# Kernel optimization log

Hardware: AMD Instinct MI355X
Metric: run time of the kernel (lower is better)

## Reference

```python
import jax, jax.numpy as jnp
import numpy as np

B, S, E = 2, 2048, 1024
N_HEADS = 16
HEAD_DIM = E // N_HEADS  # 64
ATTN_SCALE = 1.0 / np.sqrt(E)  # NOTE: original scales by 1/sqrt(hidden_dim_phi), not head_dim
ROPE_BASE = 10000.0


def _rope(t):
    # t: (B, H, S, D) with D = HEAD_DIM; interleaved-pair RoPE (torchtune-style)
    d = t.shape[-1]
    s = t.shape[-2]
    inv_freq = 1.0 / (ROPE_BASE ** (jnp.arange(0, d, 2, dtype=jnp.float32) / d))  # (D/2,)
    ang = jnp.arange(s, dtype=jnp.float32)[:, None] * inv_freq[None, :]  # (S, D/2)
    cos, sin = jnp.cos(ang), jnp.sin(ang)  # (S, D/2)
    tp = t.reshape(t.shape[:-1] + (d // 2, 2))
    te, to = tp[..., 0], tp[..., 1]  # (B,H,S,D/2)
    oe = te * cos - to * sin
    oo = te * sin + to * cos
    return jnp.stack([oe, oo], axis=-1).reshape(t.shape)


def setup_inputs() -> dict:
    key = jax.random.key(0)
    ks = jax.random.split(key, 5)
    std = 0.02
    return {
        "x": jax.random.normal(ks[0], (B, S, E), dtype=jnp.float32),
        "W_q": jax.random.normal(ks[1], (E, E), dtype=jnp.float32) * std,
        "W_k": jax.random.normal(ks[2], (E, E), dtype=jnp.float32) * std,
        "W_v": jax.random.normal(ks[3], (E, E), dtype=jnp.float32) * std,
        "W_o": jax.random.normal(ks[4], (E, E), dtype=jnp.float32) * std,
    }


def reference(x, W_q, W_k, W_v, W_o):
    b, s, e = x.shape
    hd = e // N_HEADS
    # projections -> (B, H, S, D)
    def proj(w):
        return (x @ w).reshape(b, s, N_HEADS, hd).transpose(0, 2, 1, 3)
    q = _rope(proj(W_q))
    k = _rope(proj(W_k))
    v = proj(W_v)
    scores = jnp.einsum('bhsd,bhtd->bhst', q, k) * ATTN_SCALE  # (B,H,S,S)
    causal = jnp.triu(jnp.ones((s, s), dtype=bool), k=1)
    scores = jnp.where(causal, -jnp.inf, scores)
    probs = jax.nn.softmax(scores, axis=-1)  # dropout is identity in eval mode
    out = jnp.einsum('bhst,bhtd->bhsd', probs, v)
    out = out.transpose(0, 2, 1, 3).reshape(b, s, e)
    return out @ W_o
```

## Files before the change

### kernel.cpp

```cpp
#include <hip/hip_runtime.h>
#include <hip/hip_bf16.h>

#define S_LEN 2048
#define E_DIM 1024
#define NH 16
#define HD 64
#define ATTN_SCALE 0.03125f
#define QSCALE_L2E 0.045084312f
#define KVB 128

typedef __attribute__((ext_vector_type(8))) short short8;
typedef __attribute__((ext_vector_type(8))) unsigned short ushort8;
typedef __attribute__((ext_vector_type(4))) unsigned short ushort4_t;
typedef __attribute__((ext_vector_type(4))) float f32x4;
typedef __attribute__((ext_vector_type(4))) float f4;
typedef __attribute__((ext_vector_type(2))) unsigned int uint2_t;

__device__ __forceinline__ float bf2f(unsigned short u) {
    unsigned int x = ((unsigned int)u) << 16;
    return __builtin_bit_cast(float, x);
}
__device__ __forceinline__ unsigned short f2bf(float f) {
    unsigned int x = __builtin_bit_cast(unsigned int, f);
    x += 0x7FFFu + ((x >> 16) & 1u);
    return (unsigned short)(x >> 16);
}
__device__ __forceinline__ float exp2_fast(float x) {
    float r;
    asm("v_exp_f32 %0, %1" : "=v"(r) : "v"(x));
    return r;
}
__device__ __forceinline__ void gload16(const unsigned short* g, unsigned short* l) {
    __builtin_amdgcn_global_load_lds(
        (__attribute__((address_space(1))) void*)g,
        (__attribute__((address_space(3))) void*)l, 16, 0, 0);
}

__global__ __launch_bounds__(256) void k_convert(const float* __restrict__ x,
                                                 unsigned short* __restrict__ xb) {
    size_t i = ((size_t)blockIdx.x * 256 + threadIdx.x) * 8;
    f4 a = *(const f4*)(x + i);
    f4 b = *(const f4*)(x + i + 4);
    ushort8 o;
    o[0] = f2bf(a[0]); o[1] = f2bf(a[1]); o[2] = f2bf(a[2]); o[3] = f2bf(a[3]);
    o[4] = f2bf(b[0]); o[5] = f2bf(b[1]); o[6] = f2bf(b[2]); o[7] = f2bf(b[3]);
    *(ushort8*)(xb + i) = o;
}

__global__ __launch_bounds__(256) void k_transw(const float* W0, const float* W1,
                                                const float* W2, const float* W3,
                                                unsigned short* T0, unsigned short* T1,
                                                unsigned short* T2, unsigned short* T3) {
    const float* W; unsigned short* T;
    switch (blockIdx.z) {
        case 0: W = W0; T = T0; break;
        case 1: W = W1; T = T1; break;
        case 2: W = W2; T = T2; break;
        default: W = W3; T = T3; break;
    }
    __shared__ float tile[32][33];
    int tx = threadIdx.x, ty = threadIdx.y;
    int bx = blockIdx.x * 32, by = blockIdx.y * 32;
#pragma unroll
    for (int i = 0; i < 4; i++)
        tile[ty + i * 8][tx] = W[(size_t)(by + ty + i * 8) * E_DIM + bx + tx];
    __syncthreads();
#pragma unroll
    for (int i = 0; i < 4; i++)
        T[(size_t)(bx + ty + i * 8) * E_DIM + by + tx] = f2bf(tile[tx][ty + i * 8]);
}

__global__ __launch_bounds__(256) void k_rope_table(float* __restrict__ cosT,
                                                    float* __restrict__ sinT) {
    int idx = blockIdx.x * 256 + threadIdx.x;
    int s = idx >> 5, j = idx & 31;
    float inv = expf(-(float)j * (9.210340371976184f / 32.f));
    float ang = (float)s * inv;
    cosT[idx] = cosf(ang);
    sinT[idx] = sinf(ang);
}

__global__ __launch_bounds__(256, 3)
void k_gemm97(const unsigned short* __restrict__ A,
              const unsigned short* __restrict__ B,
              unsigned short* __restrict__ Qo,
              unsigned short* __restrict__ Ko,
              unsigned short* __restrict__ Vto,
              const float* __restrict__ cosT,
              const float* __restrict__ sinT) {
    constexpr int NBN = 24;
    constexpr int NWG = 32 * NBN;
    __shared__ unsigned short Alds[4096];
    __shared__ unsigned short Blds[4096];
    int tid = threadIdx.x, lane = tid & 63, wid = tid >> 6;
    int l15 = lane & 15, lg = lane >> 4;
    int wr = wid >> 1, wc = wid & 1;
    int orig = blockIdx.y * NBN + blockIdx.x;
    int wg = (orig & 7) * (NWG / 8) + (orig >> 3);
    int bm = wg / NBN, bn = wg % NBN;
    int c0 = wid * 2, c1c = wid * 2 + 1;
    int srow0 = c0 * 16 + (lane >> 2);
    int srow1 = c1c * 16 + (lane >> 2);
    int scol = (lane & 3) * 8;
    const unsigned short* As0 = A + (size_t)(bm * 128 + srow0) * E_DIM + scol;
    const unsigned short* As1 = A + (size_t)(bm * 128 + srow1) * E_DIM + scol;
    const unsigned short* Bs0 = B + (size_t)(bn * 128 + srow0) * E_DIM + scol;
    const unsigned short* Bs1 = B + (size_t)(bn * 128 + srow1) * E_DIM + scol;
    unsigned short* Ad0 = Alds + c0 * 512;
    unsigned short* Ad1 = Alds + c1c * 512;
    unsigned short* Bd0 = Blds + c0 * 512;
    unsigned short* Bd1 = Blds + c1c * 512;
    f32x4 acc[4][4] = {};
    for (int k0 = 0; k0 < E_DIM; k0 += 32) {
        gload16(As0 + k0, Ad0);
        gload16(As1 + k0, Ad1);
        gload16(Bs0 + k0, Bd0);
        gload16(Bs1 + k0, Bd1);
        __syncthreads();
        short8 af[4], bfr[4];
#pragma unroll
        for (int mf = 0; mf < 4; mf++)
            af[mf] = *(const short8*)(Alds + (wr * 64 + mf * 16 + l15) * 32 + lg * 8);
#pragma unroll
        for (int nf = 0; nf < 4; nf++)
            bfr[nf] = *(const short8*)(Blds + (wc * 64 + nf * 16 + l15) * 32 + lg * 8);
#pragma unroll
        for (int mf = 0; mf < 4; mf++)
#pragma unroll
            for (int nf = 0; nf < 4; nf++)
                acc[mf][nf] = __builtin_amdgcn_mfma_f32_16x16x32_bf16(
                    af[mf], bfr[nf], acc[mf][nf], 0, 0, 0);
        __syncthreads();
    }
#pragma unroll
    for (int mf = 0; mf < 4; mf++) {
        int r0 = bm * 128 + wr * 64 + mf * 16 + lg * 4;
#pragma unroll
        for (int nf = 0; nf < 4; nf++) {
            int colg = bn * 128 + wc * 64 + nf * 16 + l15;
            int z = colg >> 10, c1 = colg & 1023;
            if (z == 2) {
                int h = c1 >> 6, d = c1 & 63;
                int bb = r0 >> 11, s = r0 & 2047;
                ushort4_t p;
#pragma unroll
                for (int r = 0; r < 4; r++) p[r] = f2bf(acc[mf][nf][r]);
                *(ushort4_t*)(Vto + (((size_t)((bb * 16 + h) * 64 + d)) << 11) + s) = p;
            } else {
                unsigned short* T = z ? Ko : Qo;
                int dl = c1 & 63, j = dl >> 1;
                float sgn = (dl & 1) ? 1.f : -1.f;
                float scq = z ? 1.f : QSCALE_L2E;
#pragma unroll
                for (int r = 0; r < 4; r++) {
                    int row = r0 + r, s = row & 2047;
                    float c = cosT[s * 32 + j], sn = sinT[s * 32 + j];
                    float v = acc[mf][nf][r];
                    float p = __shfl_xor(v, 1);
                    T[(size_t)row * E_DIM + c1] = f2bf((v * c + sgn * p * sn) * scq);
                }
            }
        }
    }
}

template <int BM, int BN, int NBN>
__global__ __launch_bounds__(256, 3)
void k_gemmo(const unsigned short* __restrict__ A,
             const unsigned short* __restrict__ B,
             float* __restrict__ Fo) {
    constexpr int THREADS = 256;
    constexpr int WM = BM / 2, WN = BN / 2;
    constexpr int FM = WM / 16, FN = WN / 16;
    constexpr int NT = E_DIM / 64;
    constexpr int AR = BM * 8 / THREADS;
    constexpr int BR = BN * 8 / THREADS;
    constexpr int STG = AR + BR;
    constexpr int NWG = (4096 / BM) * NBN;
    __shared__ unsigned short Al[2][BM * 64];
    __shared__ unsigned short Bl[2][BN * 64];
    int tid = threadIdx.x, lane = tid & 63, wid = tid >> 6;
    int l15 = lane & 15, lg = lane >> 4;
    int wr = wid >> 1, wc = wid & 1;
    int orig = blockIdx.y * NBN + blockIdx.x;
    int wg = (orig & 7) * (NWG / 8) + (orig >> 3);
    int bm = wg / NBN, bn = wg % NBN;

    auto stage = [&](int buf, int k0) {
#pragma unroll
        for (int i = 0; i < AR; i++) {
            int r = i * (THREADS / 8) + wid * 8 + (lane >> 3);
            int cs = (lane & 7) ^ (r & 7);
            gload16(A + (size_t)(bm * BM + r) * E_DIM + k0 + cs * 8,
                    &Al[buf][i * (THREADS * 8) + wid * 512]);
        }
#pragma unroll
        for (int i = 0; i < BR; i++) {
            int r = i * (THREADS / 8) + wid * 8 + (lane >> 3);
            int cs = (lane & 7) ^ (r & 7);
            gload16(B + (size_t)(bn * BN + r) * E_DIM + k0 + cs * 8,
                    &Bl[buf][i * (THREADS * 8) + wid * 512]);
        }
    };

    f32x4 acc[FM][FN] = {};
    stage(0, 0);
    for (int t = 0; t < NT; t++) {
        int cur = t & 1;
        if (t + 1 < NT) {
            stage(cur ^ 1, (t + 1) * 64);
            asm volatile("s_waitcnt vmcnt(%0)" :: "n"(STG) : "memory");
        } else {
            asm volatile("s_waitcnt vmcnt(0)" ::: "memory");
        }
        __builtin_amdgcn_s_barrier();
        __builtin_amdgcn_sched_barrier(0);
#pragma unroll
        for (int ks = 0; ks < 2; ks++) {
            short8 af[FM], bfv[FN];
#pragma unroll
            for (int m = 0; m < FM; m++) {
                int r = wr * WM + m * 16 + l15;
                int gc = ks * 4 + lg;
                af[m] = *(const short8*)&Al[cur][r * 64 + ((gc ^ (r & 7)) << 3)];
            }
#pragma unroll
            for (int n = 0; n < FN; n++) {
                int r = wc * WN + n * 16 + l15;
                int gc = ks * 4 + lg;
                bfv[n] = *(const short8*)&Bl[cur][r * 64 + ((gc ^ (r & 7)) << 3)];
            }
            __builtin_amdgcn_s_setprio(1);
#pragma unroll
            for (int m = 0; m < FM; m++)
#pragma unroll
                for (int n = 0; n < FN; n++)
                    acc[m][n] = __builtin_amdgcn_mfma_f32_16x16x32_bf16(
                        af[m], bfv[n], acc[m][n], 0, 0, 0);
            __builtin_amdgcn_s_setprio(0);
        }
        __builtin_amdgcn_s_barrier();
    }
#pragma unroll
    for (int m = 0; m < FM; m++) {
        int r0 = bm * BM + wr * WM + m * 16 + lg * 4;
#pragma unroll
        for (int n = 0; n < FN; n++) {
            int colg = bn * BN + wc * WN + n * 16 + l15;
#pragma unroll
            for (int r = 0; r < 4; r++)
                Fo[(size_t)(r0 + r) * E_DIM + colg] = acc[m][n][r];
        }
    }
}

__global__ __launch_bounds__(256, 2) void k_attn(const unsigned short* __restrict__ Q,
                                                 const unsigned short* __restrict__ K,
                                                 const unsigned short* __restrict__ Vt,
                                                 unsigned short* __restrict__ O) {
    __shared__ unsigned short K_lds[128 * 64];
    __shared__ unsigned short V_lds[64 * 128];
    __shared__ unsigned short P_lds[4][16][136];
    int tid = threadIdx.x, lane = tid & 63, wid = tid >> 6;
    int l15 = lane & 15, lg = lane >> 4;
    int orig = blockIdx.y * 16 + blockIdx.x;
    int wg = (orig & 7) * 64 + (orig >> 3);
    int jp = wg & 15, bh = wg >> 4;
    int b = bh >> 4, h = bh & 15;
    const size_t base_qk = (size_t)b * S_LEN * E_DIM + (size_t)h * HD;
    const unsigned short* Vbh = Vt + ((size_t)(bh * 64) << 11);

    auto stageK = [&](int kt) {
        const unsigned short* Kb = K + base_qk + (size_t)(kt * KVB) * E_DIM;
#pragma unroll
        for (int i = 0; i < 4; i++) {
            int r = i * 32 + wid * 8 + (lane >> 3);
            int cs = (lane & 7) ^ (r & 7);
            gload16(Kb + (size_t)r * E_DIM + cs * 8, K_lds + i * 2048 + wid * 512);
        }
    };
    auto stageV = [&](int kt) {
#pragma unroll
        for (int i = 0; i < 4; i++) {
            int r = i * 16 + wid * 4 + (lane >> 4);
            int cs = (lane & 15) ^ (r & 7);
            gload16(Vbh + (size_t)r * 2048 + kt * KVB + cs * 8,
                    V_lds + i * 2048 + wid * 512);
        }
    };

    for (int pass = 0; pass < 2; ++pass) {
        int qt = pass ? (31 - jp) : jp;
        const unsigned short* Qb = Q + base_qk + (size_t)(qt * 64 + wid * 16) * E_DIM;
        short8 bq[2];
#pragma unroll
        for (int s2 = 0; s2 < 2; s2++)
            bq[s2] = *(const short8*)(Qb + (size_t)l15 * E_DIM + s2 * 32 + lg * 8);
        f32x4 acc_o[4] = {};
        float m_i = -1e30f, l_i = 0.f;
        int q_glob = qt * 64 + wid * 16 + l15;
        int nkt = (qt + 2) >> 1;
        stageK(0);
        stageV(0);
        asm volatile("s_waitcnt vmcnt(4)" ::: "memory");
        __builtin_amdgcn_s_barrier();
        __builtin_amdgcn_sched_barrier(0);
        for (int kt = 0; kt < nkt; ++kt) {
            f32x4 acc_s[8] = {};
            __builtin_amdgcn_s_setprio(1);
#pragma unroll
            for (int mf = 0; mf < 8; mf++) {
                int rK = mf * 16 + l15;
#pragma unroll
                for (int s2 = 0; s2 < 2; s2++) {
                    int gc = s2 * 4 + lg;
                    short8 a = *(const short8*)&K_lds[rK * 64 + ((gc ^ (rK & 7)) << 3)];
                    acc_s[mf] = __builtin_amdgcn_mfma_f32_16x16x32_bf16(
                        a, bq[s2], acc_s[mf], 0, 0, 0);
                }
            }
            __builtin_amdgcn_s_setprio(0);
            __builtin_amdgcn_s_barrier();
            if (kt + 1 < nkt) stageK(kt + 1);
            float sv[32];
            float vmax = -1e30f;
            if (kt == nkt - 1) {
#pragma unroll
                for (int mf = 0; mf < 8; mf++)
#pragma unroll
                    for (int r = 0; r < 4; r++) {
                        int kg = kt * KVB + mf * 16 + lg * 4 + r;
                        float v = acc_s[mf][r];
                        if (kg > q_glob) v = -1e30f;
                        sv[mf * 4 + r] = v;
                        vmax = fmaxf(vmax, v);
                    }
            } else {
#pragma unroll
                for (int mf = 0; mf < 8; mf++)
#pragma unroll
                    for (int r = 0; r < 4; r++) {
                        float v = acc_s[mf][r];
                        sv[mf * 4 + r] = v;
                        vmax = fmaxf(vmax, v);
                    }
            }
            vmax = fmaxf(vmax, __shfl_xor(vmax, 16));
            vmax = fmaxf(vmax, __shfl_xor(vmax, 32));
            float m_new = fmaxf(m_i, vmax);
            float corr = exp2_fast(m_i - m_new);
            float rowsum = 0.f;
#pragma unroll
            for (int i = 0; i < 32; i++) {
                float p = exp2_fast(sv[i] - m_new);
                sv[i] = p;
                rowsum += p;
            }
            rowsum += __shfl_xor(rowsum, 16);
            rowsum += __shfl_xor(rowsum, 32);
            l_i = l_i * corr + rowsum;
            m_i = m_new;
#pragma unroll
            for (int mf = 0; mf < 8; mf++) {
                unsigned int w0, w1;
                asm("v_cvt_pk_bf16_f32 %0, %1, %2"
                    : "=v"(w0) : "v"(sv[mf * 4 + 0]), "v"(sv[mf * 4 + 1]));
                asm("v_cvt_pk_bf16_f32 %0, %1, %2"
                    : "=v"(w1) : "v"(sv[mf * 4 + 2]), "v"(sv[mf * 4 + 3]));
                uint2_t w; w[0] = w0; w[1] = w1;
                *(uint2_t*)&P_lds[wid][l15][mf * 16 + lg * 4] = w;
            }
#pragma unroll
            for (int r = 0; r < 4; r++) {
                float c4 = __shfl(corr, lg * 4 + r);
#pragma unroll
                for (int nf = 0; nf < 4; nf++) acc_o[nf][r] *= c4;
            }
            if (kt + 1 < nkt)
                asm volatile("s_waitcnt vmcnt(4)" ::: "memory");
            else
                asm volatile("s_waitcnt vmcnt(0)" ::: "memory");
            __builtin_amdgcn_s_barrier();
            __builtin_amdgcn_sched_barrier(0);
            __builtin_amdgcn_s_setprio(1);
#pragma unroll
            for (int s2 = 0; s2 < 4; s2++) {
                short8 pa = *(const short8*)&P_lds[wid][l15][s2 * 32 + lg * 8];
#pragma unroll
                for (int nf = 0; nf < 4; nf++) {
                    int rV = nf * 16 + l15;
                    int gc = s2 * 4 + lg;
                    short8 bv = *(const short8*)&V_lds[rV * 128 + ((gc ^ (rV & 7)) << 3)];
                    acc_o[nf] = __builtin_amdgcn_mfma_f32_16x16x32_bf16(
                        pa, bv, acc_o[nf], 0, 0, 0);
                }
            }
            __builtin_amdgcn_s_setprio(0);
            __builtin_amdgcn_s_barrier();
            if (kt + 1 < nkt) {
                stageV(kt + 1);
                asm volatile("s_waitcnt vmcnt(4)" ::: "memory");
            }
            __builtin_amdgcn_s_barrier();
            __builtin_amdgcn_sched_barrier(0);
        }
        unsigned short* Ob = O + base_qk + (size_t)(qt * 64 + wid * 16) * E_DIM;
#pragma unroll
        for (int r = 0; r < 4; r++) {
            float linv = 1.f / __shfl(l_i, lg * 4 + r);
#pragma unroll
            for (int nf = 0; nf < 4; nf++)
                Ob[(size_t)(lg * 4 + r) * E_DIM + nf * 16 + l15] =
                    f2bf(acc_o[nf][r] * linv);
        }
    }
}

extern "C" void kernel_launch(void* const* d_in, const int* in_sizes, int n_in,
                              void* d_out, int out_size, void* d_ws, size_t ws_size,
                              hipStream_t stream) {
    (void)in_sizes; (void)n_in; (void)out_size; (void)ws_size;
    const float* x  = (const float*)d_in[0];
    const float* Wq = (const float*)d_in[1];
    const float* Wk = (const float*)d_in[2];
    const float* Wv = (const float*)d_in[3];
    const float* Wo = (const float*)d_in[4];

    unsigned short* us = (unsigned short*)d_ws;
    unsigned short* xb    = us;
    unsigned short* WqkvT = us + 4194304;
    unsigned short* WoT   = us + 7340032;
    unsigned short* Qb    = us + 8388608;
    unsigned short* Kb    = us + 12582912;
    unsigned short* Vt    = us + 16777216;
    unsigned short* AO    = us + 20971520;
    float* cosT = (float*)((char*)d_ws + 50331648);
    float* sinT = cosT + 65536;

    k_convert<<<2048, 256, 0, stream>>>(x, xb);
    k_transw<<<dim3(32, 32, 4), dim3(32, 8), 0, stream>>>(
        Wq, Wk, Wv, Wo, WqkvT, WqkvT + 1048576, WqkvT + 2097152, WoT);
    k_rope_table<<<256, 256, 0, stream>>>(cosT, sinT);
    k_gemm97<<<dim3(24, 32), 256, 0, stream>>>(xb, WqkvT, Qb, Kb, Vt, cosT, sinT);
    k_attn<<<dim3(16, 32), 256, 0, stream>>>(Qb, Kb, Vt, AO);
    k_gemmo<128, 64, 16><<<dim3(16, 32), 256, 0, stream>>>(AO, WoT, (float*)d_out);
}
```

Baseline: 107.5 us.

## Merge prep kernels and restructure attention into per-wave 32-key pipelined tiles

Three preprocessing kernels (x convert, rope table, weight transpose) are merged into one launch to cut launch overhead. The QKV GEMM epilogue now writes V in a pre-packed MFMA-fragment layout, so the new attention kernel can load V straight into registers instead of staging it through LDS. Attention becomes one q-tile per workgroup with 32-key blocks per wave, a 3-slot per-wave K ring and double-buffered V registers. Block-wide barriers are dropped and occupancy rises to 3 blocks per CU, at the cost of smaller MFMA batches and more loop iterations.

```diff
diff --git a/kernel.cpp b/kernel.cpp
--- a/kernel.cpp
+++ b/kernel.cpp
@@ -7,7 +7,6 @@
 #define HD 64
 #define ATTN_SCALE 0.03125f
 #define QSCALE_L2E 0.045084312f
-#define KVB 128
 
 typedef __attribute__((ext_vector_type(8))) short short8;
 typedef __attribute__((ext_vector_type(8))) unsigned short ushort8;
@@ -36,48 +35,51 @@
         (__attribute__((address_space(3))) void*)l, 16, 0, 0);
 }
 
-__global__ __launch_bounds__(256) void k_convert(const float* __restrict__ x,
-                                                 unsigned short* __restrict__ xb) {
-    size_t i = ((size_t)blockIdx.x * 256 + threadIdx.x) * 8;
-    f4 a = *(const f4*)(x + i);
-    f4 b = *(const f4*)(x + i + 4);
-    ushort8 o;
-    o[0] = f2bf(a[0]); o[1] = f2bf(a[1]); o[2] = f2bf(a[2]); o[3] = f2bf(a[3]);
-    o[4] = f2bf(b[0]); o[5] = f2bf(b[1]); o[6] = f2bf(b[2]); o[7] = f2bf(b[3]);
-    *(ushort8*)(xb + i) = o;
-}
-
-__global__ __launch_bounds__(256) void k_transw(const float* W0, const float* W1,
-                                                const float* W2, const float* W3,
-                                                unsigned short* T0, unsigned short* T1,
-                                                unsigned short* T2, unsigned short* T3) {
-    const float* W; unsigned short* T;
-    switch (blockIdx.z) {
-        case 0: W = W0; T = T0; break;
-        case 1: W = W1; T = T1; break;
-        case 2: W = W2; T = T2; break;
-        default: W = W3; T = T3; break;
-    }
-    __shared__ float tile[32][33];
-    int tx = threadIdx.x, ty = threadIdx.y;
-    int bx = blockIdx.x * 32, by = blockIdx.y * 32;
-#pragma unroll
-    for (int i = 0; i < 4; i++)
-        tile[ty + i * 8][tx] = W[(size_t)(by + ty + i * 8) * E_DIM + bx + tx];
-    __syncthreads();
-#pragma unroll
-    for (int i = 0; i < 4; i++)
-        T[(size_t)(bx + ty + i * 8) * E_DIM + by + tx] = f2bf(tile[tx][ty + i * 8]);
-}
-
-__global__ __launch_bounds__(256) void k_rope_table(float* __restrict__ cosT,
-                                                    float* __restrict__ sinT) {
-    int idx = blockIdx.x * 256 + threadIdx.x;
-    int s = idx >> 5, j = idx & 31;
-    float inv = expf(-(float)j * (9.210340371976184f / 32.f));
-    float ang = (float)s * inv;
-    cosT[idx] = cosf(ang);
-    sinT[idx] = sinf(ang);
+__global__ __launch_bounds__(256) void k_prep(const float* __restrict__ x,
+                                              unsigned short* __restrict__ xb,
+                                              const float* W0, const float* W1,
+                                              const float* W2, const float* W3,
+                                              unsigned short* Tqkv,
+                                              unsigned short* Twout,
+                                              float* __restrict__ cosT,
+                                              float* __restrict__ sinT) {
+    int bid = blockIdx.x;
+    int tid = threadIdx.x;
+    if (bid < 2048) {
+        size_t i = ((size_t)bid * 256 + tid) * 8;
+        f4 a = *(const f4*)(x + i);
+        f4 b = *(const f4*)(x + i + 4);
+        ushort8 o;
+        o[0] = f2bf(a[0]); o[1] = f2bf(a[1]); o[2] = f2bf(a[2]); o[3] = f2bf(a[3]);
+        o[4] = f2bf(b[0]); o[5] = f2bf(b[1]); o[6] = f2bf(b[2]); o[7] = f2bf(b[3]);
+        *(ushort8*)(xb + i) = o;
+    } else if (bid < 2304) {
+        int idx = (bid - 2048) * 256 + tid;
+        int s = idx >> 5, j = idx & 31;
+        float inv = expf(-(float)j * (9.210340371976184f / 32.f));
+        float ang = (float)s * inv;
+        cosT[idx] = cosf(ang);
+        sinT[idx] = sinf(ang);
+    } else {
+        int t = bid - 2304;
+        int bx = (t & 31) * 32, by = ((t >> 5) & 31) * 32, z = t >> 10;
+        const float* W; unsigned short* T;
+        switch (z) {
+            case 0: W = W0; T = Tqkv; break;
+            case 1: W = W1; T = Tqkv + 1048576; break;
+            case 2: W = W2; T = Tqkv + 2097152; break;
+            default: W = W3; T = Twout; break;
+        }
+        __shared__ float tile[32][33];
+        int tx = tid & 31, ty = tid >> 5;
+#pragma unroll
+        for (int i = 0; i < 4; i++)
+            tile[ty + i * 8][tx] = W[(size_t)(by + ty + i * 8) * E_DIM + bx + tx];
+        __syncthreads();
+#pragma unroll
+        for (int i = 0; i < 4; i++)
+            T[(size_t)(bx + ty + i * 8) * E_DIM + by + tx] = f2bf(tile[tx][ty + i * 8]);
+    }
 }
 
 __global__ __launch_bounds__(256, 3)
@@ -85,7 +87,7 @@
               const unsigned short* __restrict__ B,
               unsigned short* __restrict__ Qo,
               unsigned short* __restrict__ Ko,
-              unsigned short* __restrict__ Vto,
+              unsigned short* __restrict__ VPo,
               const float* __restrict__ cosT,
               const float* __restrict__ sinT) {
     constexpr int NBN = 24;
@@ -142,10 +144,16 @@
             if (z == 2) {
                 int h = c1 >> 6, d = c1 & 63;
                 int bb = r0 >> 11, s = r0 & 2047;
+                int bh2 = bb * 16 + h;
+                int kt = s >> 5;
+                int nfv = d >> 4;
+                int lanev = (d & 15) | (((s & 31) >> 3) << 4);
+                size_t off = ((size_t)((bh2 * 64 + kt) * 4 + nfv)) * 512 +
+                             (size_t)lanev * 8 + (s & 7);
                 ushort4_t p;
 #pragma unroll
                 for (int r = 0; r < 4; r++) p[r] = f2bf(acc[mf][nf][r]);
-                *(ushort4_t*)(Vto + (((size_t)((bb * 16 + h) * 64 + d)) << 11) + s) = p;
+                *(ushort4_t*)(VPo + off) = p;
             } else {
                 unsigned short* T = z ? Ko : Qo;
                 int dl = c1 & 63, j = dl >> 1;
@@ -254,165 +262,152 @@
     }
 }
 
-__global__ __launch_bounds__(256, 2) void k_attn(const unsigned short* __restrict__ Q,
-                                                 const unsigned short* __restrict__ K,
-                                                 const unsigned short* __restrict__ Vt,
-                                                 unsigned short* __restrict__ O) {
-    __shared__ unsigned short K_lds[128 * 64];
-    __shared__ unsigned short V_lds[64 * 128];
-    __shared__ unsigned short P_lds[4][16][136];
+__global__ __launch_bounds__(256, 3)
+void k_attn8(const unsigned short* __restrict__ Q,
+             const unsigned short* __restrict__ K,
+             const unsigned short* __restrict__ VP,
+             unsigned short* __restrict__ O) {
+    __shared__ unsigned short K_lds[4][3][2048];
+    __shared__ unsigned short P_lds[4][16][36];
     int tid = threadIdx.x, lane = tid & 63, wid = tid >> 6;
     int l15 = lane & 15, lg = lane >> 4;
-    int orig = blockIdx.y * 16 + blockIdx.x;
-    int wg = (orig & 7) * 64 + (orig >> 3);
-    int jp = wg & 15, bh = wg >> 4;
+    int orig = blockIdx.y * 32 + blockIdx.x;
+    int xcd = orig & 7, idx = orig >> 3;
+    int bh = xcd * 4 + (idx & 3);
+    int qt = 31 - ((idx >> 2) & 31);
     int b = bh >> 4, h = bh & 15;
     const size_t base_qk = (size_t)b * S_LEN * E_DIM + (size_t)h * HD;
-    const unsigned short* Vbh = Vt + ((size_t)(bh * 64) << 11);
-
-    auto stageK = [&](int kt) {
-        const unsigned short* Kb = K + base_qk + (size_t)(kt * KVB) * E_DIM;
+    const unsigned short* VPb = VP + (size_t)bh * 131072;
+    unsigned short* Kw = &K_lds[wid][0][0];
+
+    int qbase = qt * 64 + wid * 16;
+    int q_glob = qbase + l15;
+    int nkt = ((qbase + 15) >> 5) + 1;
+
+    const unsigned short* Qb = Q + base_qk + (size_t)qbase * E_DIM;
+    short8 bq[2];
+#pragma unroll
+    for (int s2 = 0; s2 < 2; s2++)
+        bq[s2] = *(const short8*)(Qb + (size_t)l15 * E_DIM + s2 * 32 + lg * 8);
+
+    auto stageK = [&](int ring, int kt) {
+        const unsigned short* Kb = K + base_qk + (size_t)(kt * 32) * E_DIM;
 #pragma unroll
         for (int i = 0; i < 4; i++) {
-            int r = i * 32 + wid * 8 + (lane >> 3);
+            int r = i * 8 + (lane >> 3);
             int cs = (lane & 7) ^ (r & 7);
-            gload16(Kb + (size_t)r * E_DIM + cs * 8, K_lds + i * 2048 + wid * 512);
+            gload16(Kb + (size_t)r * E_DIM + cs * 8, Kw + ring * 2048 + i * 512);
         }
     };
-    auto stageV = [&](int kt) {
-#pragma unroll
-        for (int i = 0; i < 4; i++) {
-            int r = i * 16 + wid * 4 + (lane >> 4);
-            int cs = (lane & 15) ^ (r & 7);
-            gload16(Vbh + (size_t)r * 2048 + kt * KVB + cs * 8,
-                    V_lds + i * 2048 + wid * 512);
-        }
+    auto loadV = [&](int kt, short8 (&vv)[4]) {
+        const unsigned short* vb = VPb + (size_t)kt * 2048;
+#pragma unroll
+        for (int nf = 0; nf < 4; nf++)
+            vv[nf] = *(const short8*)(vb + (nf * 64 + lane) * 8);
     };
 
-    for (int pass = 0; pass < 2; ++pass) {
-        int qt = pass ? (31 - jp) : jp;
-        const unsigned short* Qb = Q + base_qk + (size_t)(qt * 64 + wid * 16) * E_DIM;
-        short8 bq[2];
-#pragma unroll
-        for (int s2 = 0; s2 < 2; s2++)
-            bq[s2] = *(const short8*)(Qb + (size_t)l15 * E_DIM + s2 * 32 + lg * 8);
-        f32x4 acc_o[4] = {};
-        float m_i = -1e30f, l_i = 0.f;
-        int q_glob = qt * 64 + wid * 16 + l15;
-        int nkt = (qt + 2) >> 1;
-        stageK(0);
-        stageV(0);
-        asm volatile("s_waitcnt vmcnt(4)" ::: "memory");
-        __builtin_amdgcn_s_barrier();
-        __builtin_amdgcn_sched_barrier(0);
-        for (int kt = 0; kt < nkt; ++kt) {
-            f32x4 acc_s[8] = {};
-            __builtin_amdgcn_s_setprio(1);
-#pragma unroll
-            for (int mf = 0; mf < 8; mf++) {
-                int rK = mf * 16 + l15;
-#pragma unroll
-                for (int s2 = 0; s2 < 2; s2++) {
-                    int gc = s2 * 4 + lg;
-                    short8 a = *(const short8*)&K_lds[rK * 64 + ((gc ^ (rK & 7)) << 3)];
-                    acc_s[mf] = __builtin_amdgcn_mfma_f32_16x16x32_bf16(
-                        a, bq[s2], acc_s[mf], 0, 0, 0);
+    f32x4 acc_o[4] = {};
+    float m_i = -1e30f, l_i = 0.f;
+    short8 vA[4], vB[4];
+
+    auto body = [&](int kt, short8 (&vCur)[4], short8 (&vNxt)[4]) {
+        if (kt + 1 < nkt)
+            asm volatile("s_waitcnt vmcnt(8)" ::: "memory");
+        else
+            asm volatile("s_waitcnt vmcnt(4)" ::: "memory");
+        const unsigned short* Kb = Kw + (kt % 3) * 2048;
+        f32x4 acc_s[2] = {};
+        __builtin_amdgcn_s_setprio(1);
+#pragma unroll
+        for (int mf = 0; mf < 2; mf++) {
+            int rK = mf * 16 + l15;
+#pragma unroll
+            for (int s2 = 0; s2 < 2; s2++) {
+                int gc = s2 * 4 + lg;
+                short8 a = *(const short8*)&Kb[rK * 64 + ((gc ^ (rK & 7)) << 3)];
+                acc_s[mf] = __builtin_amdgcn_mfma_f32_16x16x32_bf16(
+                    a, bq[s2], acc_s[mf], 0, 0, 0);
+            }
+        }
+        __builtin_amdgcn_s_setprio(0);
+        float sv[8];
+        float vmax = -1e30f;
+        bool domask = (kt + 2 >= nkt);
+#pragma unroll
+        for (int mf = 0; mf < 2; mf++)
+#pragma unroll
+            for (int r = 0; r < 4; r++) {
+                float v = acc_s[mf][r];
+                if (domask) {
+                    int kg = kt * 32 + mf * 16 + lg * 4 + r;
+                    if (kg > q_glob) v = -1e30f;
                 }
+                sv[mf * 4 + r] = v;
+                vmax = fmaxf(vmax, v);
             }
-            __builtin_amdgcn_s_setprio(0);
-            __builtin_amdgcn_s_barrier();
-            if (kt + 1 < nkt) stageK(kt + 1);
-            float sv[32];
-            float vmax = -1e30f;
-            if (kt == nkt - 1) {
-#pragma unroll
-                for (int mf = 0; mf < 8; mf++)
-#pragma unroll
-                    for (int r = 0; r < 4; r++) {
-                        int kg = kt * KVB + mf * 16 + lg * 4 + r;
-                        float v = acc_s[mf][r];
-                        if (kg > q_glob) v = -1e30f;
-                        sv[mf * 4 + r] = v;
-                        vmax = fmaxf(vmax, v);
-                    }
-            } else {
-#pragma unroll
-                for (int mf = 0; mf < 8; mf++)
-#pragma unroll
-                    for (int r = 0; r < 4; r++) {
-                        float v = acc_s[mf][r];
-                        sv[mf * 4 + r] = v;
-                        vmax = fmaxf(vmax, v);
-                    }
-            }
-            vmax = fmaxf(vmax, __shfl_xor(vmax, 16));
-            vmax = fmaxf(vmax, __shfl_xor(vmax, 32));
-            float m_new = fmaxf(m_i, vmax);
-            float corr = exp2_fast(m_i - m_new);
-            float rowsum = 0.f;
-#pragma unroll
-            for (int i = 0; i < 32; i++) {
-                float p = exp2_fast(sv[i] - m_new);
-                sv[i] = p;
-                rowsum += p;
-            }
-            rowsum += __shfl_xor(rowsum, 16);
-            rowsum += __shfl_xor(rowsum, 32);
-            l_i = l_i * corr + rowsum;
-            m_i = m_new;
-#pragma unroll
-            for (int mf = 0; mf < 8; mf++) {
-                unsigned int w0, w1;
-                asm("v_cvt_pk_bf16_f32 %0, %1, %2"
-                    : "=v"(w0) : "v"(sv[mf * 4 + 0]), "v"(sv[mf * 4 + 1]));
-                asm("v_cvt_pk_bf16_f32 %0, %1, %2"
-                    : "=v"(w1) : "v"(sv[mf * 4 + 2]), "v"(sv[mf * 4 + 3]));
-                uint2_t w; w[0] = w0; w[1] = w1;
-                *(uint2_t*)&P_lds[wid][l15][mf * 16 + lg * 4] = w;
-            }
-#pragma unroll
-            for (int r = 0; r < 4; r++) {
-                float c4 = __shfl(corr, lg * 4 + r);
-#pragma unroll
-                for (int nf = 0; nf < 4; nf++) acc_o[nf][r] *= c4;
-            }
-            if (kt + 1 < nkt)
-                asm volatile("s_waitcnt vmcnt(4)" ::: "memory");
-            else
-                asm volatile("s_waitcnt vmcnt(0)" ::: "memory");
-            __builtin_amdgcn_s_barrier();
-            __builtin_amdgcn_sched_barrier(0);
-            __builtin_amdgcn_s_setprio(1);
-#pragma unroll
-            for (int s2 = 0; s2 < 4; s2++) {
-                short8 pa = *(const short8*)&P_lds[wid][l15][s2 * 32 + lg * 8];
-#pragma unroll
-                for (int nf = 0; nf < 4; nf++) {
-                    int rV = nf * 16 + l15;
-                    int gc = s2 * 4 + lg;
-                    short8 bv = *(const short8*)&V_lds[rV * 128 + ((gc ^ (rV & 7)) << 3)];
-                    acc_o[nf] = __builtin_amdgcn_mfma_f32_16x16x32_bf16(
-                        pa, bv, acc_o[nf], 0, 0, 0);
-                }
-            }
-            __builtin_amdgcn_s_setprio(0);
-            __builtin_amdgcn_s_barrier();
-            if (kt + 1 < nkt) {
-                stageV(kt + 1);
-                asm volatile("s_waitcnt vmcnt(4)" ::: "memory");
-            }
-            __builtin_amdgcn_s_barrier();
-            __builtin_amdgcn_sched_barrier(0);
-        }
-        unsigned short* Ob = O + base_qk + (size_t)(qt * 64 + wid * 16) * E_DIM;
+        vmax = fmaxf(vmax, __shfl_xor(vmax, 16));
+        vmax = fmaxf(vmax, __shfl_xor(vmax, 32));
+        float m_new = fmaxf(m_i, vmax);
+        float corr = exp2_fast(m_i - m_new);
+        float rowsum = 0.f;
+#pragma unroll
+        for (int i = 0; i < 8; i++) {
+            float p = exp2_fast(sv[i] - m_new);
+            sv[i] = p;
+            rowsum += p;
+        }
+        rowsum += __shfl_xor(rowsum, 16);
+        rowsum += __shfl_xor(rowsum, 32);
+        l_i = l_i * corr + rowsum;
+        m_i = m_new;
+#pragma unroll
+        for (int mf = 0; mf < 2; mf++) {
+            unsigned int w0, w1;
+            asm("v_cvt_pk_bf16_f32 %0, %1, %2"
+                : "=v"(w0) : "v"(sv[mf * 4 + 0]), "v"(sv[mf * 4 + 1]));
+            asm("v_cvt_pk_bf16_f32 %0, %1, %2"
+                : "=v"(w1) : "v"(sv[mf * 4 + 2]), "v"(sv[mf * 4 + 3]));
+            uint2_t w; w[0] = w0; w[1] = w1;
+            *(uint2_t*)&P_lds[wid][l15][mf * 16 + lg * 4] = w;
+        }
 #pragma unroll
         for (int r = 0; r < 4; r++) {
-            float linv = 1.f / __shfl(l_i, lg * 4 + r);
-#pragma unroll
-            for (int nf = 0; nf < 4; nf++)
-                Ob[(size_t)(lg * 4 + r) * E_DIM + nf * 16 + l15] =
-                    f2bf(acc_o[nf][r] * linv);
-        }
+            float c4 = __shfl(corr, lg * 4 + r);
+#pragma unroll
+            for (int nf = 0; nf < 4; nf++) acc_o[nf][r] *= c4;
+        }
+        if (kt + 1 < nkt)
+            asm volatile("s_waitcnt vmcnt(4)" ::: "memory");
+        else
+            asm volatile("s_waitcnt vmcnt(0)" ::: "memory");
+        short8 pa = *(const short8*)&P_lds[wid][l15][lg * 8];
+        __builtin_amdgcn_s_setprio(1);
+#pragma unroll
+        for (int nf = 0; nf < 4; nf++)
+            acc_o[nf] = __builtin_amdgcn_mfma_f32_16x16x32_bf16(
+                pa, vCur[nf], acc_o[nf], 0, 0, 0);
+        __builtin_amdgcn_s_setprio(0);
+        if (kt + 1 < nkt) loadV(kt + 1, vNxt);
+        if (kt + 2 < nkt) stageK((kt + 2) % 3, kt + 2);
+    };
+
+    stageK(0, 0);
+    loadV(0, vA);
+    if (nkt > 1) stageK(1, 1);
+    int kt = 0;
+    while (kt < nkt) {
+        body(kt, vA, vB); kt++;
+        if (kt < nkt) { body(kt, vB, vA); kt++; }
+    }
+
+    unsigned short* Ob = O + base_qk + (size_t)qbase * E_DIM;
+#pragma unroll
+    for (int r = 0; r < 4; r++) {
+        float linv = 1.f / __shfl(l_i, lg * 4 + r);
+#pragma unroll
+        for (int nf = 0; nf < 4; nf++)
+            Ob[(size_t)(lg * 4 + r) * E_DIM + nf * 16 + l15] =
+                f2bf(acc_o[nf][r] * linv);
     }
 }
 
@@ -432,16 +427,13 @@
     unsigned short* WoT   = us + 7340032;
     unsigned short* Qb    = us + 8388608;
     unsigned short* Kb    = us + 12582912;
-    unsigned short* Vt    = us + 16777216;
+    unsigned short* VP    = us + 16777216;
     unsigned short* AO    = us + 20971520;
     float* cosT = (float*)((char*)d_ws + 50331648);
     float* sinT = cosT + 65536;
 
-    k_convert<<<2048, 256, 0, stream>>>(x, xb);
-    k_transw<<<dim3(32, 32, 4), dim3(32, 8), 0, stream>>>(
-        Wq, Wk, Wv, Wo, WqkvT, WqkvT + 1048576, WqkvT + 2097152, WoT);
-    k_rope_table<<<256, 256, 0, stream>>>(cosT, sinT);
-    k_gemm97<<<dim3(24, 32), 256, 0, stream>>>(xb, WqkvT, Qb, Kb, Vt, cosT, sinT);
-    k_attn<<<dim3(16, 32), 256, 0, stream>>>(Qb, Kb, Vt, AO);
+    k_prep<<<6400, 256, 0, stream>>>(x, xb, Wq, Wk, Wv, Wo, WqkvT, WoT, cosT, sinT);
+    k_gemm97<<<dim3(24, 32), 256, 0, stream>>>(xb, WqkvT, Qb, Kb, VP, cosT, sinT);
+    k_attn8<<<dim3(32, 32), 256, 0, stream>>>(Qb, Kb, VP, AO);
     k_gemmo<128, 64, 16><<<dim3(16, 32), 256, 0, stream>>>(AO, WoT, (float*)d_out);
 }
```

Result: slower. 118.7 us (+10.4%).

## Fuse prep kernels, widen GEMM K-step with swizzled LDS, split attention grid per q-tile

Applied to the files above, without the earlier changes.

The three preprocessing kernels (x conversion, RoPE table, weight transpose) become one launch that dispatches on block index, which removes two kernel launches. The QKV GEMM now stages 64-wide K tiles into an XOR-swizzled LDS layout, halving the barrier count and setting MFMA priority. Attention no longer pairs two q-tiles per block: each block handles one q-tile, the grid is doubled, heavy tiles are scheduled first, blocks are grouped by XCD, and occupancy is raised to 3. This trades the balanced pairing for more, smaller blocks plus a tighter register budget.

```diff
diff --git a/kernel.cpp b/kernel.cpp
--- a/kernel.cpp
+++ b/kernel.cpp
@@ -36,48 +36,51 @@
         (__attribute__((address_space(3))) void*)l, 16, 0, 0);
 }
 
-__global__ __launch_bounds__(256) void k_convert(const float* __restrict__ x,
-                                                 unsigned short* __restrict__ xb) {
-    size_t i = ((size_t)blockIdx.x * 256 + threadIdx.x) * 8;
-    f4 a = *(const f4*)(x + i);
-    f4 b = *(const f4*)(x + i + 4);
-    ushort8 o;
-    o[0] = f2bf(a[0]); o[1] = f2bf(a[1]); o[2] = f2bf(a[2]); o[3] = f2bf(a[3]);
-    o[4] = f2bf(b[0]); o[5] = f2bf(b[1]); o[6] = f2bf(b[2]); o[7] = f2bf(b[3]);
-    *(ushort8*)(xb + i) = o;
-}
-
-__global__ __launch_bounds__(256) void k_transw(const float* W0, const float* W1,
-                                                const float* W2, const float* W3,
-                                                unsigned short* T0, unsigned short* T1,
-                                                unsigned short* T2, unsigned short* T3) {
-    const float* W; unsigned short* T;
-    switch (blockIdx.z) {
-        case 0: W = W0; T = T0; break;
-        case 1: W = W1; T = T1; break;
-        case 2: W = W2; T = T2; break;
-        default: W = W3; T = T3; break;
-    }
-    __shared__ float tile[32][33];
-    int tx = threadIdx.x, ty = threadIdx.y;
-    int bx = blockIdx.x * 32, by = blockIdx.y * 32;
-#pragma unroll
-    for (int i = 0; i < 4; i++)
-        tile[ty + i * 8][tx] = W[(size_t)(by + ty + i * 8) * E_DIM + bx + tx];
-    __syncthreads();
-#pragma unroll
-    for (int i = 0; i < 4; i++)
-        T[(size_t)(bx + ty + i * 8) * E_DIM + by + tx] = f2bf(tile[tx][ty + i * 8]);
-}
-
-__global__ __launch_bounds__(256) void k_rope_table(float* __restrict__ cosT,
-                                                    float* __restrict__ sinT) {
-    int idx = blockIdx.x * 256 + threadIdx.x;
-    int s = idx >> 5, j = idx & 31;
-    float inv = expf(-(float)j * (9.210340371976184f / 32.f));
-    float ang = (float)s * inv;
-    cosT[idx] = cosf(ang);
-    sinT[idx] = sinf(ang);
+__global__ __launch_bounds__(256) void k_prep(const float* __restrict__ x,
+                                              unsigned short* __restrict__ xb,
+                                              const float* W0, const float* W1,
+                                              const float* W2, const float* W3,
+                                              unsigned short* Tqkv,
+                                              unsigned short* Twout,
+                                              float* __restrict__ cosT,
+                                              float* __restrict__ sinT) {
+    int bid = blockIdx.x;
+    int tid = threadIdx.x;
+    if (bid < 2048) {
+        size_t i = ((size_t)bid * 256 + tid) * 8;
+        f4 a = *(const f4*)(x + i);
+        f4 b = *(const f4*)(x + i + 4);
+        ushort8 o;
+        o[0] = f2bf(a[0]); o[1] = f2bf(a[1]); o[2] = f2bf(a[2]); o[3] = f2bf(a[3]);
+        o[4] = f2bf(b[0]); o[5] = f2bf(b[1]); o[6] = f2bf(b[2]); o[7] = f2bf(b[3]);
+        *(ushort8*)(xb + i) = o;
+    } else if (bid < 2304) {
+        int idx = (bid - 2048) * 256 + tid;
+        int s = idx >> 5, j = idx & 31;
+        float inv = expf(-(float)j * (9.210340371976184f / 32.f));
+        float ang = (float)s * inv;
+        cosT[idx] = cosf(ang);
+        sinT[idx] = sinf(ang);
+    } else {
+        int t = bid - 2304;
+        int bx = (t & 31) * 32, by = ((t >> 5) & 31) * 32, z = t >> 10;
+        const float* W; unsigned short* T;
+        switch (z) {
+            case 0: W = W0; T = Tqkv; break;
+            case 1: W = W1; T = Tqkv + 1048576; break;
+            case 2: W = W2; T = Tqkv + 2097152; break;
+            default: W = W3; T = Twout; break;
+        }
+        __shared__ float tile[32][33];
+        int tx = tid & 31, ty = tid >> 5;
+#pragma unroll
+        for (int i = 0; i < 4; i++)
+            tile[ty + i * 8][tx] = W[(size_t)(by + ty + i * 8) * E_DIM + bx + tx];
+        __syncthreads();
+#pragma unroll
+        for (int i = 0; i < 4; i++)
+            T[(size_t)(bx + ty + i * 8) * E_DIM + by + tx] = f2bf(tile[tx][ty + i * 8]);
+    }
 }
 
 __global__ __launch_bounds__(256, 3)
@@ -90,46 +93,56 @@
               const float* __restrict__ sinT) {
     constexpr int NBN = 24;
     constexpr int NWG = 32 * NBN;
-    __shared__ unsigned short Alds[4096];
-    __shared__ unsigned short Blds[4096];
+    __shared__ unsigned short Alds[128 * 64];
+    __shared__ unsigned short Blds[128 * 64];
     int tid = threadIdx.x, lane = tid & 63, wid = tid >> 6;
     int l15 = lane & 15, lg = lane >> 4;
     int wr = wid >> 1, wc = wid & 1;
     int orig = blockIdx.y * NBN + blockIdx.x;
     int wg = (orig & 7) * (NWG / 8) + (orig >> 3);
     int bm = wg / NBN, bn = wg % NBN;
-    int c0 = wid * 2, c1c = wid * 2 + 1;
-    int srow0 = c0 * 16 + (lane >> 2);
-    int srow1 = c1c * 16 + (lane >> 2);
-    int scol = (lane & 3) * 8;
-    const unsigned short* As0 = A + (size_t)(bm * 128 + srow0) * E_DIM + scol;
-    const unsigned short* As1 = A + (size_t)(bm * 128 + srow1) * E_DIM + scol;
-    const unsigned short* Bs0 = B + (size_t)(bn * 128 + srow0) * E_DIM + scol;
-    const unsigned short* Bs1 = B + (size_t)(bn * 128 + srow1) * E_DIM + scol;
-    unsigned short* Ad0 = Alds + c0 * 512;
-    unsigned short* Ad1 = Alds + c1c * 512;
-    unsigned short* Bd0 = Blds + c0 * 512;
-    unsigned short* Bd1 = Blds + c1c * 512;
+
     f32x4 acc[4][4] = {};
-    for (int k0 = 0; k0 < E_DIM; k0 += 32) {
-        gload16(As0 + k0, Ad0);
-        gload16(As1 + k0, Ad1);
-        gload16(Bs0 + k0, Bd0);
-        gload16(Bs1 + k0, Bd1);
+    for (int k0 = 0; k0 < E_DIM; k0 += 64) {
+#pragma unroll
+        for (int i = 0; i < 4; i++) {
+            int r = wid * 32 + i * 8 + (lane >> 3);
+            int cs = (lane & 7) ^ (r & 7);
+            gload16(A + (size_t)(bm * 128 + r) * E_DIM + k0 + cs * 8,
+                    Alds + (wid * 256 + i * 64) * 8);
+        }
+#pragma unroll
+        for (int i = 0; i < 4; i++) {
+            int r = wid * 32 + i * 8 + (lane >> 3);
+            int cs = (lane & 7) ^ (r & 7);
+            gload16(B + (size_t)(bn * 128 + r) * E_DIM + k0 + cs * 8,
+                    Blds + (wid * 256 + i * 64) * 8);
+        }
         __syncthreads();
-        short8 af[4], bfr[4];
-#pragma unroll
-        for (int mf = 0; mf < 4; mf++)
-            af[mf] = *(const short8*)(Alds + (wr * 64 + mf * 16 + l15) * 32 + lg * 8);
-#pragma unroll
-        for (int nf = 0; nf < 4; nf++)
-            bfr[nf] = *(const short8*)(Blds + (wc * 64 + nf * 16 + l15) * 32 + lg * 8);
-#pragma unroll
-        for (int mf = 0; mf < 4; mf++)
-#pragma unroll
-            for (int nf = 0; nf < 4; nf++)
-                acc[mf][nf] = __builtin_amdgcn_mfma_f32_16x16x32_bf16(
-                    af[mf], bfr[nf], acc[mf][nf], 0, 0, 0);
+#pragma unroll
+        for (int ks = 0; ks < 2; ks++) {
+            short8 af[4], bfr[4];
+#pragma unroll
+            for (int mf = 0; mf < 4; mf++) {
+                int r = wr * 64 + mf * 16 + l15;
+                int gc = ks * 4 + lg;
+                af[mf] = *(const short8*)(Alds + r * 64 + ((gc ^ (r & 7)) << 3));
+            }
+#pragma unroll
+            for (int nf = 0; nf < 4; nf++) {
+                int r = wc * 64 + nf * 16 + l15;
+                int gc = ks * 4 + lg;
+                bfr[nf] = *(const short8*)(Blds + r * 64 + ((gc ^ (r & 7)) << 3));
+            }
+            __builtin_amdgcn_s_setprio(1);
+#pragma unroll
+            for (int mf = 0; mf < 4; mf++)
+#pragma unroll
+                for (int nf = 0; nf < 4; nf++)
+                    acc[mf][nf] = __builtin_amdgcn_mfma_f32_16x16x32_bf16(
+                        af[mf], bfr[nf], acc[mf][nf], 0, 0, 0);
+            __builtin_amdgcn_s_setprio(0);
+        }
         __syncthreads();
     }
 #pragma unroll
@@ -254,7 +267,7 @@
     }
 }
 
-__global__ __launch_bounds__(256, 2) void k_attn(const unsigned short* __restrict__ Q,
+__global__ __launch_bounds__(256, 3) void k_attn(const unsigned short* __restrict__ Q,
                                                  const unsigned short* __restrict__ K,
                                                  const unsigned short* __restrict__ Vt,
                                                  unsigned short* __restrict__ O) {
@@ -263,9 +276,10 @@
     __shared__ unsigned short P_lds[4][16][136];
     int tid = threadIdx.x, lane = tid & 63, wid = tid >> 6;
     int l15 = lane & 15, lg = lane >> 4;
-    int orig = blockIdx.y * 16 + blockIdx.x;
-    int wg = (orig & 7) * 64 + (orig >> 3);
-    int jp = wg & 15, bh = wg >> 4;
+    int orig = blockIdx.y * 32 + blockIdx.x;
+    int xcd = orig & 7, idx = orig >> 3;
+    int bh = xcd * 4 + (idx & 3);
+    int qt = 31 - ((idx >> 2) & 31);
     int b = bh >> 4, h = bh & 15;
     const size_t base_qk = (size_t)b * S_LEN * E_DIM + (size_t)h * HD;
     const unsigned short* Vbh = Vt + ((size_t)(bh * 64) << 11);
@@ -289,130 +303,127 @@
         }
     };
 
-    for (int pass = 0; pass < 2; ++pass) {
-        int qt = pass ? (31 - jp) : jp;
-        const unsigned short* Qb = Q + base_qk + (size_t)(qt * 64 + wid * 16) * E_DIM;
-        short8 bq[2];
-#pragma unroll
-        for (int s2 = 0; s2 < 2; s2++)
-            bq[s2] = *(const short8*)(Qb + (size_t)l15 * E_DIM + s2 * 32 + lg * 8);
-        f32x4 acc_o[4] = {};
-        float m_i = -1e30f, l_i = 0.f;
-        int q_glob = qt * 64 + wid * 16 + l15;
-        int nkt = (qt + 2) >> 1;
-        stageK(0);
-        stageV(0);
-        asm volatile("s_waitcnt vmcnt(4)" ::: "memory");
+    const unsigned short* Qb = Q + base_qk + (size_t)(qt * 64 + wid * 16) * E_DIM;
+    short8 bq[2];
+#pragma unroll
+    for (int s2 = 0; s2 < 2; s2++)
+        bq[s2] = *(const short8*)(Qb + (size_t)l15 * E_DIM + s2 * 32 + lg * 8);
+    f32x4 acc_o[4] = {};
+    float m_i = -1e30f, l_i = 0.f;
+    int q_glob = qt * 64 + wid * 16 + l15;
+    int nkt = (qt + 2) >> 1;
+    stageK(0);
+    stageV(0);
+    asm volatile("s_waitcnt vmcnt(4)" ::: "memory");
+    __builtin_amdgcn_s_barrier();
+    __builtin_amdgcn_sched_barrier(0);
+    for (int kt = 0; kt < nkt; ++kt) {
+        f32x4 acc_s[8] = {};
+        __builtin_amdgcn_s_setprio(1);
+#pragma unroll
+        for (int mf = 0; mf < 8; mf++) {
+            int rK = mf * 16 + l15;
+#pragma unroll
+            for (int s2 = 0; s2 < 2; s2++) {
+                int gc = s2 * 4 + lg;
+                short8 a = *(const short8*)&K_lds[rK * 64 + ((gc ^ (rK & 7)) << 3)];
+                acc_s[mf] = __builtin_amdgcn_mfma_f32_16x16x32_bf16(
+                    a, bq[s2], acc_s[mf], 0, 0, 0);
+            }
+        }
+        __builtin_amdgcn_s_setprio(0);
+        __builtin_amdgcn_s_barrier();
+        if (kt + 1 < nkt) stageK(kt + 1);
+        float sv[32];
+        float vmax = -1e30f;
+        if (kt == nkt - 1) {
+#pragma unroll
+            for (int mf = 0; mf < 8; mf++)
+#pragma unroll
+                for (int r = 0; r < 4; r++) {
+                    int kg = kt * KVB + mf * 16 + lg * 4 + r;
+                    float v = acc_s[mf][r];
+                    if (kg > q_glob) v = -1e30f;
+                    sv[mf * 4 + r] = v;
+                    vmax = fmaxf(vmax, v);
+                }
+        } else {
+#pragma unroll
+            for (int mf = 0; mf < 8; mf++)
+#pragma unroll
+                for (int r = 0; r < 4; r++) {
+                    float v = acc_s[mf][r];
+                    sv[mf * 4 + r] = v;
+                    vmax = fmaxf(vmax, v);
+                }
+        }
+        vmax = fmaxf(vmax, __shfl_xor(vmax, 16));
+        vmax = fmaxf(vmax, __shfl_xor(vmax, 32));
+        float m_new = fmaxf(m_i, vmax);
+        float corr = exp2_fast(m_i - m_new);
+        float rowsum = 0.f;
+#pragma unroll
+        for (int i = 0; i < 32; i++) {
+            float p = exp2_fast(sv[i] - m_new);
+            sv[i] = p;
+            rowsum += p;
+        }
+        rowsum += __shfl_xor(rowsum, 16);
+        rowsum += __shfl_xor(rowsum, 32);
+        l_i = l_i * corr + rowsum;
+        m_i = m_new;
+#pragma unroll
+        for (int mf = 0; mf < 8; mf++) {
+            unsigned int w0, w1;
+            asm("v_cvt_pk_bf16_f32 %0, %1, %2"
+                : "=v"(w0) : "v"(sv[mf * 4 + 0]), "v"(sv[mf * 4 + 1]));
+            asm("v_cvt_pk_bf16_f32 %0, %1, %2"
+                : "=v"(w1) : "v"(sv[mf * 4 + 2]), "v"(sv[mf * 4 + 3]));
+            uint2_t w; w[0] = w0; w[1] = w1;
+            *(uint2_t*)&P_lds[wid][l15][mf * 16 + lg * 4] = w;
+        }
+#pragma unroll
+        for (int r = 0; r < 4; r++) {
+            float c4 = __shfl(corr, lg * 4 + r);
+#pragma unroll
+            for (int nf = 0; nf < 4; nf++) acc_o[nf][r] *= c4;
+        }
+        if (kt + 1 < nkt)
+            asm volatile("s_waitcnt vmcnt(4)" ::: "memory");
+        else
+            asm volatile("s_waitcnt vmcnt(0)" ::: "memory");
         __builtin_amdgcn_s_barrier();
         __builtin_amdgcn_sched_barrier(0);
-        for (int kt = 0; kt < nkt; ++kt) {
-            f32x4 acc_s[8] = {};
-            __builtin_amdgcn_s_setprio(1);
-#pragma unroll
-            for (int mf = 0; mf < 8; mf++) {
-                int rK = mf * 16 + l15;
-#pragma unroll
-                for (int s2 = 0; s2 < 2; s2++) {
-                    int gc = s2 * 4 + lg;
-                    short8 a = *(const short8*)&K_lds[rK * 64 + ((gc ^ (rK & 7)) << 3)];
-                    acc_s[mf] = __builtin_amdgcn_mfma_f32_16x16x32_bf16(
-                        a, bq[s2], acc_s[mf], 0, 0, 0);
-                }
-            }
-            __builtin_amdgcn_s_setprio(0);
-            __builtin_amdgcn_s_barrier();
-            if (kt + 1 < nkt) stageK(kt + 1);
-            float sv[32];
-            float vmax = -1e30f;
-            if (kt == nkt - 1) {
-#pragma unroll
-                for (int mf = 0; mf < 8; mf++)
-#pragma unroll
-                    for (int r = 0; r < 4; r++) {
-                        int kg = kt * KVB + mf * 16 + lg * 4 + r;
-                        float v = acc_s[mf][r];
-                        if (kg > q_glob) v = -1e30f;
-                        sv[mf * 4 + r] = v;
-                        vmax = fmaxf(vmax, v);
-                    }
-            } else {
-#pragma unroll
-                for (int mf = 0; mf < 8; mf++)
-#pragma unroll
-                    for (int r = 0; r < 4; r++) {
-                        float v = acc_s[mf][r];
-                        sv[mf * 4 + r] = v;
-                        vmax = fmaxf(vmax, v);
-                    }
-            }
-            vmax = fmaxf(vmax, __shfl_xor(vmax, 16));
-            vmax = fmaxf(vmax, __shfl_xor(vmax, 32));
-            float m_new = fmaxf(m_i, vmax);
-            float corr = exp2_fast(m_i - m_new);
-            float rowsum = 0.f;
-#pragma unroll
-            for (int i = 0; i < 32; i++) {
-                float p = exp2_fast(sv[i] - m_new);
-                sv[i] = p;
-                rowsum += p;
-            }
-            rowsum += __shfl_xor(rowsum, 16);
-            rowsum += __shfl_xor(rowsum, 32);
-            l_i = l_i * corr + rowsum;
-            m_i = m_new;
-#pragma unroll
-            for (int mf = 0; mf < 8; mf++) {
-                unsigned int w0, w1;
-                asm("v_cvt_pk_bf16_f32 %0, %1, %2"
-                    : "=v"(w0) : "v"(sv[mf * 4 + 0]), "v"(sv[mf * 4 + 1]));
-                asm("v_cvt_pk_bf16_f32 %0, %1, %2"
-                    : "=v"(w1) : "v"(sv[mf * 4 + 2]), "v"(sv[mf * 4 + 3]));
-                uint2_t w; w[0] = w0; w[1] = w1;
-                *(uint2_t*)&P_lds[wid][l15][mf * 16 + lg * 4] = w;
-            }
-#pragma unroll
-            for (int r = 0; r < 4; r++) {
-                float c4 = __shfl(corr, lg * 4 + r);
-#pragma unroll
-                for (int nf = 0; nf < 4; nf++) acc_o[nf][r] *= c4;
-            }
-            if (kt + 1 < nkt)
-                asm volatile("s_waitcnt vmcnt(4)" ::: "memory");
-            else
-                asm volatile("s_waitcnt vmcnt(0)" ::: "memory");
-            __builtin_amdgcn_s_barrier();
-            __builtin_amdgcn_sched_barrier(0);
-            __builtin_amdgcn_s_setprio(1);
-#pragma unroll
-            for (int s2 = 0; s2 < 4; s2++) {
-                short8 pa = *(const short8*)&P_lds[wid][l15][s2 * 32 + lg * 8];
-#pragma unroll
-                for (int nf = 0; nf < 4; nf++) {
-                    int rV = nf * 16 + l15;
-                    int gc = s2 * 4 + lg;
-                    short8 bv = *(const short8*)&V_lds[rV * 128 + ((gc ^ (rV & 7)) << 3)];
-                    acc_o[nf] = __builtin_amdgcn_mfma_f32_16x16x32_bf16(
-                        pa, bv, acc_o[nf], 0, 0, 0);
-                }
-            }
-            __builtin_amdgcn_s_setprio(0);
-            __builtin_amdgcn_s_barrier();
-            if (kt + 1 < nkt) {
-                stageV(kt + 1);
-                asm volatile("s_waitcnt vmcnt(4)" ::: "memory");
-            }
-            __builtin_amdgcn_s_barrier();
-            __builtin_amdgcn_sched_barrier(0);
-        }
-        unsigned short* Ob = O + base_qk + (size_t)(qt * 64 + wid * 16) * E_DIM;
-#pragma unroll
-        for (int r = 0; r < 4; r++) {
-            float linv = 1.f / __shfl(l_i, lg * 4 + r);
-#pragma unroll
-            for (int nf = 0; nf < 4; nf++)
-                Ob[(size_t)(lg * 4 + r) * E_DIM + nf * 16 + l15] =
-                    f2bf(acc_o[nf][r] * linv);
-        }
+        __builtin_amdgcn_s_setprio(1);
+#pragma unroll
+        for (int s2 = 0; s2 < 4; s2++) {
+            short8 pa = *(const short8*)&P_lds[wid][l15][s2 * 32 + lg * 8];
+#pragma unroll
+            for (int nf = 0; nf < 4; nf++) {
+                int rV = nf * 16 + l15;
+                int gc = s2 * 4 + lg;
+                short8 bv = *(const short8*)&V_lds[rV * 128 + ((gc ^ (rV & 7)) << 3)];
+                acc_o[nf] = __builtin_amdgcn_mfma_f32_16x16x32_bf16(
+                    pa, bv, acc_o[nf], 0, 0, 0);
+            }
+        }
+        __builtin_amdgcn_s_setprio(0);
+        __builtin_amdgcn_s_barrier();
+        if (kt + 1 < nkt) {
+            stageV(kt + 1);
+            asm volatile("s_waitcnt vmcnt(4)" ::: "memory");
+        }
+        __builtin_amdgcn_s_barrier();
+        __builtin_amdgcn_sched_barrier(0);
+    }
+    unsigned short* Ob = O + base_qk + (size_t)(qt * 64 + wid * 16) * E_DIM;
+#pragma unroll
+    for (int r = 0; r < 4; r++) {
+        float linv = 1.f / __shfl(l_i, lg * 4 + r);
+#pragma unroll
+        for (int nf = 0; nf < 4; nf++)
+            Ob[(size_t)(lg * 4 + r) * E_DIM + nf * 16 + l15] =
+                f2bf(acc_o[nf][r] * linv);
     }
 }
 
@@ -437,11 +448,8 @@
     float* cosT = (float*)((char*)d_ws + 50331648);
     float* sinT = cosT + 65536;
 
-    k_convert<<<2048, 256, 0, stream>>>(x, xb);
-    k_transw<<<dim3(32, 32, 4), dim3(32, 8), 0, stream>>>(
-        Wq, Wk, Wv, Wo, WqkvT, WqkvT + 1048576, WqkvT + 2097152, WoT);
-    k_rope_table<<<256, 256, 0, stream>>>(cosT, sinT);
+    k_prep<<<6400, 256, 0, stream>>>(x, xb, Wq, Wk, Wv, Wo, WqkvT, WoT, cosT, sinT);
     k_gemm97<<<dim3(24, 32), 256, 0, stream>>>(xb, WqkvT, Qb, Kb, Vt, cosT, sinT);
-    k_attn<<<dim3(16, 32), 256, 0, stream>>>(Qb, Kb, Vt, AO);
+    k_attn<<<dim3(32, 32), 256, 0, stream>>>(Qb, Kb, Vt, AO);
     k_gemmo<128, 64, 16><<<dim3(16, 32), 256, 0, stream>>>(AO, WoT, (float*)d_out);
 }
```

After: 95.75 us. 1.12x faster.
